# Performance work log

Measured on AMD Instinct MI355X. Metric: run time of the kernel, lower is better.

## Reference

```python
import jax, jax.numpy as jnp
import numpy as np

HIDDEN = 2880
NUM_EXPERTS = 32
TOP_K = 4


def setup_inputs() -> dict:
    key = jax.random.key(0)
    k1, k2, k3 = jax.random.split(key, 3)
    hidden_states = jax.random.normal(k1, (4, 4096, HIDDEN), dtype=jnp.float32)
    weight = jax.random.normal(k2, (NUM_EXPERTS, HIDDEN), dtype=jnp.float32) * (1.0 / np.sqrt(HIDDEN))
    bias = jax.random.normal(k3, (NUM_EXPERTS,), dtype=jnp.float32) * 0.02
    return {"hidden_states": hidden_states, "weight": weight, "bias": bias}


def reference(hidden_states, weight, bias):
    # flatten tokens: [T, H]
    x = hidden_states.reshape(-1, HIDDEN)
    # router logits: [T, E]
    router_logits = jnp.einsum('th,eh->te', x, weight) + bias
    # top-k selection along experts
    top_vals, top_idx = jax.lax.top_k(router_logits, TOP_K)  # [T, K]
    top_vals = jax.nn.softmax(top_vals, axis=-1)
    # scatter normalized scores back into a zero [T, E] tensor
    T = router_logits.shape[0]
    rows = jnp.arange(T)[:, None]
    router_scores = jnp.zeros_like(router_logits).at[rows, top_idx].set(top_vals)
    return router_scores, top_idx
```

## Files before the change

### kernel.cpp

```cpp
#include <hip/hip_runtime.h>
#include <math.h>


#define HIDDEN 2880
#define NE 32
#define TOPK 4
#define TPB 32
#define CKF 256
#define NCH 12
#define ROWF 260
#define KS_TOT 96
#define VS (KS_TOT * 2 * 512)

typedef __attribute__((ext_vector_type(8))) short bf16x8;
typedef __attribute__((ext_vector_type(4))) float f32x4;

#define MFMA(a, b, c) __builtin_amdgcn_mfma_f32_16x16x32_bf16((a), (b), (c), 0, 0, 0)

__global__ void wb_kernel(const float* __restrict__ w, unsigned short* __restrict__ wb) {
    int i = blockIdx.x * 256 + threadIdx.x;
    if (i >= 3 * VS) return;
    int j = i & 7;
    int t = i >> 3;
    int l = t & 63;  t >>= 6;
    int et = t & 1;  t >>= 1;
    int ks = t % KS_TOT;
    int ver = t / KS_TOT;
    unsigned short outv = 0;
    int k = -1;
    if (ks < 88)       k = ks * 32 + (l >> 4) * 8 + j;
    else if (ks >= 94) k = 2624 + (ks - 88) * 32 + (l >> 4) * 8 + j;
    if (k >= 0) {
        int e = et * 16 + (l & 15);
        float v = w[e * HIDDEN + k];
        unsigned u = __float_as_uint(v);
        unsigned h = u >> 16;
        float r = v - __uint_as_float(u & 0xffff0000u);
        unsigned ur = __float_as_uint(r);
        unsigned m = ur >> 16;
        float r2 = r - __uint_as_float(ur & 0xffff0000u);
        unsigned lo = __float_as_uint(r2) >> 16;
        outv = (unsigned short)(ver == 0 ? h : (ver == 1 ? m : lo));
    }
    wb[i] = outv;
}

__device__ __forceinline__ void split24(float4 a, float4 b,
                                        bf16x8& H, bf16x8& M, bf16x8& L) {
    union { bf16x8 v; unsigned u[4]; } h, m, l;
    float f[8] = {a.x, a.y, a.z, a.w, b.x, b.y, b.z, b.w};
    unsigned hh[8], mm[8], ll[8];
#pragma unroll
    for (int i = 0; i < 8; ++i) {
        unsigned u = __float_as_uint(f[i]);
        hh[i] = u >> 16;
        float r = f[i] - __uint_as_float(u & 0xffff0000u);
        unsigned ur = __float_as_uint(r);
        mm[i] = ur >> 16;
        float r2 = r - __uint_as_float(ur & 0xffff0000u);
        ll[i] = __float_as_uint(r2) >> 16;
    }
#pragma unroll
    for (int i = 0; i < 4; ++i) {
        h.u[i] = hh[2 * i] | (hh[2 * i + 1] << 16);
        m.u[i] = mm[2 * i] | (mm[2 * i + 1] << 16);
        l.u[i] = ll[2 * i] | (ll[2 * i + 1] << 16);
    }
    H = h.v; M = m.v; L = l.v;
}

__global__ __launch_bounds__(512, 4)
void router_kernel(const float* __restrict__ x,
                   const unsigned short* __restrict__ wb,
                   const float* __restrict__ bias,
                   float* __restrict__ out_scores,
                   float* __restrict__ out_idx)
{
    __shared__ float buf[2][TPB][ROWF];

    const int tid  = threadIdx.x;
    const int lane = tid & 63;
    const int w    = tid >> 6;
    const int tl   = lane & 15;
    const int kg   = lane >> 4;
    const int tok0 = blockIdx.x * TPB;

    const float* xsr = x + (size_t)(tok0 + 4 * w) * HIDDEN + lane * 4;
    const unsigned short* wk = wb + lane * 8;

    f32x4 acc0 = {0.f, 0.f, 0.f, 0.f};
    f32x4 acc1 = {0.f, 0.f, 0.f, 0.f};
    f32x4 acc2 = {0.f, 0.f, 0.f, 0.f};
    f32x4 acc3 = {0.f, 0.f, 0.f, 0.f};

    float4 ga0, ga1, ga2, ga3, gb0, gb1, gb2, gb3;

#define GLOAD(g0_, g1_, g2_, g3_, c) do {                                         \
    const int ko_ = ((c) < 11 ? (c) * CKF : 2624);                                \
    g0_ = *(const float4*)(xsr + ko_);                                            \
    g1_ = *(const float4*)(xsr + (size_t)HIDDEN + ko_);                           \
    g2_ = *(const float4*)(xsr + (size_t)2 * HIDDEN + ko_);                       \
    g3_ = *(const float4*)(xsr + (size_t)3 * HIDDEN + ko_);                       \
} while (0)

#define SWRITE(b, g0_, g1_, g2_, g3_) do {                                        \
    float* d_ = &buf[b][4 * w][0] + lane * 4;                                     \
    *(float4*)(d_)            = g0_;                                              \
    *(float4*)(d_ + ROWF)     = g1_;                                              \
    *(float4*)(d_ + 2 * ROWF) = g2_;                                              \
    *(float4*)(d_ + 3 * ROWF) = g3_;                                              \
} while (0)

#define BAR() do {                                                                \
    asm volatile("s_waitcnt lgkmcnt(0)" ::: "memory");                            \
    __builtin_amdgcn_s_barrier();                                                 \
} while (0)

#define COMPUTE(b, c) do {                                                        \
    const unsigned short* p_ = wk + (size_t)(8 * (c) + w) * 1024;                 \
    bf16x8 W0 = *(const bf16x8*)(p_);                                             \
    bf16x8 W1 = *(const bf16x8*)(p_ + 512);                                       \
    bf16x8 W2 = *(const bf16x8*)(p_ + VS);                                        \
    bf16x8 W3 = *(const bf16x8*)(p_ + VS + 512);                                  \
    bf16x8 W4 = *(const bf16x8*)(p_ + 2 * VS);                                    \
    bf16x8 W5 = *(const bf16x8*)(p_ + 2 * VS + 512);                              \
    const int xo_ = w * 32 + kg * 8;                                              \
    float4 a0_ = *(const float4*)(&buf[b][tl][xo_]);                              \
    float4 a1_ = *(const float4*)(&buf[b][tl][xo_ + 4]);                          \
    bf16x8 xh_, xm_, xl_;                                                         \
    split24(a0_, a1_, xh_, xm_, xl_);                                             \
    acc0 = MFMA(W0, xh_, acc0);  acc1 = MFMA(W1, xh_, acc1);                      \
    acc0 = MFMA(W2, xh_, acc0);  acc1 = MFMA(W3, xh_, acc1);                      \
    acc0 = MFMA(W4, xh_, acc0);  acc1 = MFMA(W5, xh_, acc1);                      \
    acc0 = MFMA(W0, xm_, acc0);  acc1 = MFMA(W1, xm_, acc1);                      \
    acc0 = MFMA(W2, xm_, acc0);  acc1 = MFMA(W3, xm_, acc1);                      \
    acc0 = MFMA(W0, xl_, acc0);  acc1 = MFMA(W1, xl_, acc1);                      \
    float4 b0_ = *(const float4*)(&buf[b][16 + tl][xo_]);                         \
    float4 b1_ = *(const float4*)(&buf[b][16 + tl][xo_ + 4]);                     \
    split24(b0_, b1_, xh_, xm_, xl_);                                             \
    acc2 = MFMA(W0, xh_, acc2);  acc3 = MFMA(W1, xh_, acc3);                      \
    acc2 = MFMA(W2, xh_, acc2);  acc3 = MFMA(W3, xh_, acc3);                      \
    acc2 = MFMA(W4, xh_, acc2);  acc3 = MFMA(W5, xh_, acc3);                      \
    acc2 = MFMA(W0, xm_, acc2);  acc3 = MFMA(W1, xm_, acc3);                      \
    acc2 = MFMA(W2, xm_, acc2);  acc3 = MFMA(W3, xm_, acc3);                      \
    acc2 = MFMA(W0, xl_, acc2);  acc3 = MFMA(W1, xl_, acc3);                      \
} while (0)

    GLOAD(ga0, ga1, ga2, ga3, 0);
    GLOAD(gb0, gb1, gb2, gb3, 1);
    SWRITE(0, ga0, ga1, ga2, ga3);
    GLOAD(ga0, ga1, ga2, ga3, 2);
    BAR();

#pragma unroll 1
    for (int i = 0; i < 6; ++i) {
        const int c0 = 2 * i;
        SWRITE(1, gb0, gb1, gb2, gb3);
        if (i < 5) GLOAD(gb0, gb1, gb2, gb3, c0 + 3);
        COMPUTE(0, c0);
        BAR();
        if (i < 5) SWRITE(0, ga0, ga1, ga2, ga3);
        if (i < 4) GLOAD(ga0, ga1, ga2, ga3, c0 + 4);
        COMPUTE(1, c0 + 1);
        BAR();
    }

#undef GLOAD
#undef SWRITE
#undef BAR
#undef COMPUTE

    __syncthreads();

    float* pool = &buf[0][0][0];
#define PART(p, t, e) pool[((p) * TPB + (t)) * 36 + (e)]
    {
        const int eb = kg * 4;
        *(f32x4*)&PART(w, tl, eb)       = acc0;
        *(f32x4*)&PART(w, tl, 16 + eb)  = acc1;
        *(f32x4*)&PART(w, 16 + tl, eb)      = acc2;
        *(f32x4*)&PART(w, 16 + tl, 16 + eb) = acc3;
    }
    __syncthreads();

    float* score = pool + 8 * TPB * 36;
    if (tid < TPB) {
        float lg[NE];
#pragma unroll
        for (int e = 0; e < NE; ++e) {
            float s = bias[e];
#pragma unroll
            for (int p = 0; p < 8; ++p) s += PART(p, tid, e);
            lg[e] = s;
        }

        float vals[TOPK]; int idxs[TOPK]; unsigned chosen = 0u;
#pragma unroll
        for (int k = 0; k < TOPK; ++k) {
            float m = -INFINITY; int mi = 0;
#pragma unroll
            for (int e = 0; e < NE; ++e) {
                const bool take = (((chosen >> e) & 1u) == 0u) && (lg[e] > m);
                m  = take ? lg[e] : m;
                mi = take ? e : mi;
            }
            vals[k] = m; idxs[k] = mi; chosen |= (1u << (unsigned)mi);
        }
        const float mx = vals[0];
        float p[TOPK]; float sum = 0.f;
#pragma unroll
        for (int k = 0; k < TOPK; ++k) { p[k] = __expf(vals[k] - mx); sum += p[k]; }
        const float inv = 1.0f / sum;
#pragma unroll
        for (int e = 0; e < NE; ++e) {
            float v = 0.f;
#pragma unroll
            for (int k = 0; k < TOPK; ++k) v = (e == idxs[k]) ? p[k] * inv : v;
            score[tid * 33 + e] = v;
        }
        const int t = tok0 + tid;
        float4 iv = make_float4((float)idxs[0], (float)idxs[1], (float)idxs[2], (float)idxs[3]);
        *reinterpret_cast<float4*>(out_idx + (size_t)t * TOPK) = iv;
    }
    __syncthreads();

    {
        const int f = tid * 2;
        const int t = f >> 5, e = f & 31;
        float2 v = make_float2(score[t * 33 + e], score[t * 33 + e + 1]);
        *reinterpret_cast<float2*>(out_scores + (size_t)blockIdx.x * TPB * NE + f) = v;
    }
#undef PART
}

extern "C" void kernel_launch(void* const* d_in, const int* in_sizes, int n_in,
                              void* d_out, int out_size, void* d_ws, size_t ws_size,
                              hipStream_t stream)
{
    const float* x = (const float*)d_in[0];
    const float* w = (const float*)d_in[1];
    const float* b = (const float*)d_in[2];
    const int T = in_sizes[0] / HIDDEN;

    unsigned short* wbuf = (unsigned short*)d_ws;
    float* out        = (float*)d_out;
    float* out_scores = out;
    float* out_idx    = out + (size_t)T * NE;

    wb_kernel<<<dim3((3 * VS + 255) / 256), dim3(256), 0, stream>>>(w, wbuf);
    router_kernel<<<dim3(T / TPB), dim3(512), 0, stream>>>(x, wbuf, b, out_scores, out_idx);
}
```

Baseline: 50.20 us.

## Stage activations via direct global-to-LDS loads with XOR-swizzled layout

Replaces the register-staged global loads plus LDS stores with __builtin_amdgcn_global_load_lds, which writes x tiles straight into shared memory. Row padding is replaced by an XOR swizzle on the 16-byte column index to avoid bank conflicts. The loop becomes a single 12-chunk double-buffered pipeline synchronised with vmcnt waits and barriers. This removes VGPR pressure and the LDS write instructions, at the cost of an extra barrier per chunk and relying on vmcnt ordering for correctness.

```diff
diff --git a/kernel.cpp b/kernel.cpp
--- a/kernel.cpp
+++ b/kernel.cpp
@@ -7,13 +7,13 @@
 #define TOPK 4
 #define TPB 32
 #define CKF 256
-#define NCH 12
-#define ROWF 260
 #define KS_TOT 96
 #define VS (KS_TOT * 2 * 512)
 
 typedef __attribute__((ext_vector_type(8))) short bf16x8;
 typedef __attribute__((ext_vector_type(4))) float f32x4;
+typedef __attribute__((address_space(3))) unsigned int LU;
+typedef __attribute__((address_space(1))) const unsigned int GU;
 
 #define MFMA(a, b, c) __builtin_amdgcn_mfma_f32_16x16x32_bf16((a), (b), (c), 0, 0, 0)
 
@@ -76,7 +76,7 @@
                    float* __restrict__ out_scores,
                    float* __restrict__ out_idx)
 {
-    __shared__ float buf[2][TPB][ROWF];
+    __shared__ float buf[2][TPB][CKF];
 
     const int tid  = threadIdx.x;
     const int lane = tid & 63;
@@ -85,7 +85,6 @@
     const int kg   = lane >> 4;
     const int tok0 = blockIdx.x * TPB;
 
-    const float* xsr = x + (size_t)(tok0 + 4 * w) * HIDDEN + lane * 4;
     const unsigned short* wk = wb + lane * 8;
 
     f32x4 acc0 = {0.f, 0.f, 0.f, 0.f};
@@ -93,27 +92,16 @@
     f32x4 acc2 = {0.f, 0.f, 0.f, 0.f};
     f32x4 acc3 = {0.f, 0.f, 0.f, 0.f};
 
-    float4 ga0, ga1, ga2, ga3, gb0, gb1, gb2, gb3;
-
-#define GLOAD(g0_, g1_, g2_, g3_, c) do {                                         \
+#define STAGEC(b, c) do {                                                         \
     const int ko_ = ((c) < 11 ? (c) * CKF : 2624);                                \
-    g0_ = *(const float4*)(xsr + ko_);                                            \
-    g1_ = *(const float4*)(xsr + (size_t)HIDDEN + ko_);                           \
-    g2_ = *(const float4*)(xsr + (size_t)2 * HIDDEN + ko_);                       \
-    g3_ = *(const float4*)(xsr + (size_t)3 * HIDDEN + ko_);                       \
-} while (0)
-
-#define SWRITE(b, g0_, g1_, g2_, g3_) do {                                        \
-    float* d_ = &buf[b][4 * w][0] + lane * 4;                                     \
-    *(float4*)(d_)            = g0_;                                              \
-    *(float4*)(d_ + ROWF)     = g1_;                                              \
-    *(float4*)(d_ + 2 * ROWF) = g2_;                                              \
-    *(float4*)(d_ + 3 * ROWF) = g3_;                                              \
-} while (0)
-
-#define BAR() do {                                                                \
-    asm volatile("s_waitcnt lgkmcnt(0)" ::: "memory");                            \
-    __builtin_amdgcn_s_barrier();                                                 \
+    _Pragma("unroll")                                                             \
+    for (int i_ = 0; i_ < 4; ++i_) {                                              \
+        const int row_ = 4 * w + i_;                                              \
+        const float* g_ = x + (size_t)(tok0 + row_) * HIDDEN + ko_               \
+                            + ((lane ^ (row_ & 7)) << 2);                         \
+        __builtin_amdgcn_global_load_lds((GU*)g_, (LU*)&buf[b][row_][0],          \
+                                         16, 0, 0);                               \
+    }                                                                             \
 } while (0)
 
 #define COMPUTE(b, c) do {                                                        \
@@ -124,9 +112,10 @@
     bf16x8 W3 = *(const bf16x8*)(p_ + VS + 512);                                  \
     bf16x8 W4 = *(const bf16x8*)(p_ + 2 * VS);                                    \
     bf16x8 W5 = *(const bf16x8*)(p_ + 2 * VS + 512);                              \
-    const int xo_ = w * 32 + kg * 8;                                              \
-    float4 a0_ = *(const float4*)(&buf[b][tl][xo_]);                              \
-    float4 a1_ = *(const float4*)(&buf[b][tl][xo_ + 4]);                          \
+    const int K_  = tl & 7;                          \
+    const int j0_ = w * 8 + kg * 2;                  \
+    float4 a0_ = *(const float4*)(&buf[b][tl][(j0_ ^ K_) << 2]);                  \
+    float4 a1_ = *(const float4*)(&buf[b][tl][((j0_ + 1) ^ K_) << 2]);            \
     bf16x8 xh_, xm_, xl_;                                                         \
     split24(a0_, a1_, xh_, xm_, xl_);                                             \
     acc0 = MFMA(W0, xh_, acc0);  acc1 = MFMA(W1, xh_, acc1);                      \
@@ -135,8 +124,8 @@
     acc0 = MFMA(W0, xm_, acc0);  acc1 = MFMA(W1, xm_, acc1);                      \
     acc0 = MFMA(W2, xm_, acc0);  acc1 = MFMA(W3, xm_, acc1);                      \
     acc0 = MFMA(W0, xl_, acc0);  acc1 = MFMA(W1, xl_, acc1);                      \
-    float4 b0_ = *(const float4*)(&buf[b][16 + tl][xo_]);                         \
-    float4 b1_ = *(const float4*)(&buf[b][16 + tl][xo_ + 4]);                     \
+    float4 b0_ = *(const float4*)(&buf[b][16 + tl][(j0_ ^ K_) << 2]);             \
+    float4 b1_ = *(const float4*)(&buf[b][16 + tl][((j0_ + 1) ^ K_) << 2]);       \
     split24(b0_, b1_, xh_, xm_, xl_);                                             \
     acc2 = MFMA(W0, xh_, acc2);  acc3 = MFMA(W1, xh_, acc3);                      \
     acc2 = MFMA(W2, xh_, acc2);  acc3 = MFMA(W3, xh_, acc3);                      \
@@ -146,28 +135,25 @@
     acc2 = MFMA(W0, xl_, acc2);  acc3 = MFMA(W1, xl_, acc3);                      \
 } while (0)
 
-    GLOAD(ga0, ga1, ga2, ga3, 0);
-    GLOAD(gb0, gb1, gb2, gb3, 1);
-    SWRITE(0, ga0, ga1, ga2, ga3);
-    GLOAD(ga0, ga1, ga2, ga3, 2);
-    BAR();
+    STAGEC(0, 0);
+    STAGEC(1, 1);
+    asm volatile("s_waitcnt vmcnt(4)" ::: "memory");
+    __builtin_amdgcn_s_barrier();
 
 #pragma unroll 1
-    for (int i = 0; i < 6; ++i) {
-        const int c0 = 2 * i;
-        SWRITE(1, gb0, gb1, gb2, gb3);
-        if (i < 5) GLOAD(gb0, gb1, gb2, gb3, c0 + 3);
-        COMPUTE(0, c0);
-        BAR();
-        if (i < 5) SWRITE(0, ga0, ga1, ga2, ga3);
-        if (i < 4) GLOAD(ga0, ga1, ga2, ga3, c0 + 4);
-        COMPUTE(1, c0 + 1);
-        BAR();
-    }
-
-#undef GLOAD
-#undef SWRITE
-#undef BAR
+    for (int c = 0; c < 12; ++c) {
+        COMPUTE(c & 1, c);
+        asm volatile("s_waitcnt lgkmcnt(0)" ::: "memory");
+        __builtin_amdgcn_s_barrier();
+        if (c + 2 < 12) STAGEC(c & 1, c + 2);
+        if (c + 1 < 12) {
+            if (c + 2 < 12) asm volatile("s_waitcnt vmcnt(4)" ::: "memory");
+            else            asm volatile("s_waitcnt vmcnt(0)" ::: "memory");
+            __builtin_amdgcn_s_barrier();
+        }
+    }
+
+#undef STAGEC
 #undef COMPUTE
 
     __syncthreads();
@@ -176,8 +162,8 @@
 #define PART(p, t, e) pool[((p) * TPB + (t)) * 36 + (e)]
     {
         const int eb = kg * 4;
-        *(f32x4*)&PART(w, tl, eb)       = acc0;
-        *(f32x4*)&PART(w, tl, 16 + eb)  = acc1;
+        *(f32x4*)&PART(w, tl, eb)           = acc0;
+        *(f32x4*)&PART(w, tl, 16 + eb)      = acc1;
         *(f32x4*)&PART(w, 16 + tl, eb)      = acc2;
         *(f32x4*)&PART(w, 16 + tl, 16 + eb) = acc3;
     }
```

Result: slower. 55.90 us (+11.4%).
